# Performance work log

Measured on AMD Instinct MI355X. Metric: run time of the kernel, lower is better.

## Reference

```python
import jax, jax.numpy as jnp
import numpy as np

N, E, IN_DIM, OUT_DIM, NNZ = 4096, 2048, 256, 256, 65536
ALPHA = 0.2          # LeakyReLU negative slope
NEG_GAT = -9e15      # masked_fill value for GAT adjacency mask
NEG_ATT = -1e9       # masked_fill value inside ScaledDotProductAttention_hyper


def setup_inputs() -> dict:
    key = jax.random.key(0)
    ks = jax.random.split(key, 10)
    stdv = 1.0 / np.sqrt(OUT_DIM)
    u = lambda k, shape: jax.random.uniform(k, shape, jnp.float32, -stdv, stdv)
    x = jax.random.normal(ks[0], (N, IN_DIM), jnp.float32)
    node_idx = jax.random.randint(ks[1], (NNZ,), 0, N, jnp.int32)
    edge_idx = jax.random.randint(ks[2], (NNZ,), 0, E, jnp.int32)
    hyperedge_index = jnp.stack([node_idx, edge_idx])  # [2, NNZ]
    return {
        "x": x,
        "weight": u(ks[3], (IN_DIM, OUT_DIM)),
        "weight2": u(ks[4], (IN_DIM, OUT_DIM)),
        "weight3": u(ks[5], (OUT_DIM, OUT_DIM)),
        "weight_g": u(ks[6], (IN_DIM, OUT_DIM)),
        "a_g": u(ks[7], (2 * OUT_DIM, 1)),
        "word_context": u(ks[8], (1, OUT_DIM)),
        "bias": u(ks[9], (OUT_DIM,)),
        "hyperedge_index": hyperedge_index,
        "num_edges": E,
    }


def reference(x, weight, weight2, weight3, weight_g, a_g, word_context, bias,
              hyperedge_index, num_edges):
    n = x.shape[0]
    d = weight_g.shape[1]
    temp = d ** 0.5  # temperature = out_features ** 0.5

    # --- hypergraph preprocessing: dense incidence H [N, E] and node adjacency A [N, N]
    H = jnp.zeros((n, num_edges), x.dtype).at[hyperedge_index[0], hyperedge_index[1]].set(1.0)
    A = (H @ H.T > 0).astype(x.dtype)
    A = A.at[jnp.arange(n), jnp.arange(n)].set(1.0)  # fill_diagonal_(1)

    # --- dense GAT-style attention over the clique-expanded graph
    Wh_g = x @ weight_g                               # [N, D]
    Wh1 = Wh_g @ a_g[:d]                              # [N, 1]
    Wh2 = Wh_g @ a_g[d:]                              # [N, 1]
    e_g = jax.nn.leaky_relu(Wh1 + Wh2.T, ALPHA)       # [N, N]
    attention_g = jax.nn.softmax(jnp.where(A > 0, e_g, NEG_GAT), axis=1)

    # --- project node-node attention onto hyperedges: [N, E]
    graph2hyper = attention_g @ H

    # --- dual hypergraph cross-attention (eval mode: dropout is identity)
    x_4att = x @ weight2                              # [N, D]
    xw = x @ weight + bias                            # [N, D] (transfer=True)

    # attention1: hyperedge queries attend over nodes, mask = H.T [E, N]
    q1 = jnp.broadcast_to(word_context[0], (num_edges, d))
    attn1 = (q1 / temp) @ x_4att.T                    # [E, N]
    attn1 = jnp.where(H.T == 0, NEG_ATT, attn1)
    att1 = jax.nn.softmax(graph2hyper.T, axis=-1) + jax.nn.softmax(attn1, axis=-1)
    edge = att1 @ xw                                  # [E, D]
    att2he = att1.T                                   # [N, E]

    # attention2: node queries attend over hyperedges, mask = H [N, E]
    edge_4att = edge @ weight3                        # [E, D]
    attn2 = (x_4att / temp) @ edge_4att.T             # [N, E]
    attn2 = jnp.where(H == 0, NEG_ATT, attn2)
    att2hn = jax.nn.softmax(graph2hyper, axis=-1) + jax.nn.softmax(attn2, axis=-1)
    node = att2hn @ edge                              # [N, D]

    # --- combine attentions and aggregate
    att2_he_out = att2he @ att2he.T                   # [N, N]
    att2_hn_out = att2hn @ att2hn.T                   # [N, N]
    attention_out = attention_g + att2_he_out + att2_hn_out
    h_prime_g = jax.nn.elu(attention_out @ Wh_g)      # concat=True -> ELU

    node = jax.nn.relu(node)                          # concat=True -> ReLU, then squeeze
    return node, h_prime_g
```

## Files before the change

### kernel.cpp

```cpp
#include <hip/hip_runtime.h>
#include <cstdint>
#include <cstddef>


#define DI __device__ __forceinline__
typedef unsigned short u16;
typedef unsigned char  u8;
typedef unsigned int   u32;
typedef __bf16 bf16x8 __attribute__((ext_vector_type(8)));
typedef float  f32x4  __attribute__((ext_vector_type(4)));
typedef u32    u32x4  __attribute__((ext_vector_type(4)));
typedef int    i32x4  __attribute__((ext_vector_type(4)));
typedef int    i32x8  __attribute__((ext_vector_type(8)));

constexpr int NN  = 4096;
constexpr int EE  = 2048;
constexpr int NNZb = 65536;

constexpr size_t MB = (size_t)1 << 20;
constexpr size_t OFF_HBITS   = 0;
constexpr size_t OFF_HBITST  = 1*MB;
constexpr size_t OFF_ABITS   = 2*MB;
constexpr size_t OFF_EDGE    = 2*MB;
constexpr size_t OFF_WH1     = 4*MB;
constexpr size_t OFF_WH2     = 4*MB + 16384;
constexpr size_t OFF_V       = 4*MB + 32768;
constexpr size_t OFF_RSINV   = 4*MB + 49152;
constexpr size_t OFF_WCAT    = 5*MB;
constexpr size_t OFF_XB      = 6*MB;
constexpr size_t OFF_EDGET   = 6*MB;
constexpr size_t OFF_HN2T    = 7*MB;
constexpr size_t OFF_WHG     = 8*MB;
constexpr size_t OFF_X4ATT   = 10*MB;
constexpr size_t OFF_YB      = 12*MB;
constexpr size_t OFF_XWT     = 14*MB;
constexpr size_t OFF_WHGTA   = 16*MB;
constexpr size_t OFF_HBT     = 18*MB;
constexpr size_t OFF_EDGE2T  = 18*MB;
constexpr size_t OFF_WHGTB   = 26*MB;
constexpr size_t OFF_EXPA    = 36*MB;
constexpr size_t OFF_ATT1    = 36*MB;
constexpr size_t OFF_ATT2HN  = 36*MB;
constexpr size_t OFF_ATT1T   = 52*MB;
constexpr size_t OFF_G2H     = 68*MB;
constexpr size_t OFF_G2HT    = 84*MB;
constexpr size_t OFF_ATT2HNT = 84*MB;
constexpr size_t OFF_ATTN2   = 100*MB;
constexpr size_t OFF_G1      = 116*MB;
constexpr size_t OFF_C2      = 120*MB;
constexpr size_t OFF_HN2ACC  = 124*MB;

DI u16 to_bf(float f) {
  union { float f; u32 u; } x; x.f = f;
  u32 r = x.u + 0x7fffu + ((x.u >> 16) & 1u);
  return (u16)(r >> 16);
}
DI float from_bf(u16 h) { union { u32 u; float f; } x; x.u = (u32)h << 16; return x.f; }
DI void store_bf4(u16* p, float a, float b, float c, float d) {
  u32 lo = (u32)to_bf(a) | ((u32)to_bf(b) << 16);
  u32 hi = (u32)to_bf(c) | ((u32)to_bf(d) << 16);
  *(u32*)p = lo; *((u32*)p + 1) = hi;
}
DI u32 pack_fp8x4(float a, float b, float c, float d) {
  int p = __builtin_amdgcn_cvt_pk_fp8_f32(a, b, 0, false);
  p = __builtin_amdgcn_cvt_pk_fp8_f32(c, d, p, true);
  return (u32)p;
}

DI float wredf(float v) {
  #pragma unroll
  for (int o = 32; o; o >>= 1) v += __shfl_down(v, o);
  return v;
}
DI int wredi(int v) {
  #pragma unroll
  for (int o = 32; o; o >>= 1) v += __shfl_down(v, o);
  return v;
}

typedef __attribute__((address_space(3))) void lds_void;
typedef __attribute__((address_space(1))) void glb_void;
DI void async_load16(const void* g, void* l) {
  __builtin_amdgcn_global_load_lds((glb_void*)(uintptr_t)g,
                                   (lds_void*)(u32)(uintptr_t)l, 16, 0, 0);
}

template <int BM, int BN, class Epi>
DI void gemm_body(const u16* __restrict__ A, const u16* __restrict__ B,
                  int nb, int K, int k0, int kLen, Epi epi, int tile,
                  u16* As, u16* Bs)
{
  constexpr int BK = 64;
  constexpr int WM = BM / 2, WN = BN / 2;
  constexpr int FM = WM / 16, FN = WN / 16;
  constexpr int AI = (BM * 8) / 256, BI = (BN * 8) / 256;

  const int tid = threadIdx.x;
  const int w = tid >> 6, l = tid & 63;
  const int bi = tile / nb, bj = tile - bi * nb;
  const int i0 = bi * BM, j0 = bj * BN;
  const int wm = (w & 1) * WM, wn = (w >> 1) * WN;
  const int quad = l >> 4, m16 = l & 15;

  f32x4 acc[FM][FN] = {};

  for (int kb = k0; kb < k0 + kLen; kb += BK) {
    __syncthreads();
    #pragma unroll
    for (int i = 0; i < AI; ++i) {
      const int ci = (i * 4 + w) * 64 + l;
      const int r = ci >> 3;
      const int lc = (ci & 7) ^ (r & 7);
      async_load16(A + (size_t)(i0 + r) * K + kb + lc * 8, &As[(i * 4 + w) * 512]);
    }
    #pragma unroll
    for (int i = 0; i < BI; ++i) {
      const int ci = (i * 4 + w) * 64 + l;
      const int r = ci >> 3;
      const int lc = (ci & 7) ^ (r & 7);
      async_load16(B + (size_t)(j0 + r) * K + kb + lc * 8, &Bs[(i * 4 + w) * 512]);
    }
    __syncthreads();
    #pragma unroll
    for (int ks = 0; ks < 2; ++ks) {
      bf16x8 af[FM], bfv[FN];
      #pragma unroll
      for (int mi = 0; mi < FM; ++mi) {
        const int row = wm + mi * 16 + m16;
        af[mi] = *(const bf16x8*)&As[row * BK + (((ks * 4 + quad) ^ (row & 7)) * 8)];
      }
      #pragma unroll
      for (int ni = 0; ni < FN; ++ni) {
        const int row = wn + ni * 16 + m16;
        bfv[ni] = *(const bf16x8*)&Bs[row * BK + (((ks * 4 + quad) ^ (row & 7)) * 8)];
      }
      #pragma unroll
      for (int mi = 0; mi < FM; ++mi)
        #pragma unroll
        for (int ni = 0; ni < FN; ++ni)
          acc[mi][ni] = __builtin_amdgcn_mfma_f32_16x16x32_bf16(
              af[mi], bfv[ni], acc[mi][ni], 0, 0, 0);
    }
  }
  #pragma unroll
  for (int mi = 0; mi < FM; ++mi)
    #pragma unroll
    for (int ni = 0; ni < FN; ++ni) {
      const int rb = i0 + wm + mi * 16 + quad * 4;
      const int c  = j0 + wn + ni * 16 + m16;
      epi(rb, c, acc[mi][ni]);
    }
}

DI void t32_tile(const u16* __restrict__ in, u16* __restrict__ out,
                 int R, int C, int bx, int by, u16* t) {
  int tx = threadIdx.x & 31, ty = threadIdx.x >> 5;
  int x0 = bx * 32, y0 = by * 32;
  #pragma unroll
  for (int k = 0; k < 32; k += 8)
    t[(ty + k) * 33 + tx] = in[(size_t)(y0 + ty + k) * C + x0 + tx];
  __syncthreads();
  #pragma unroll
  for (int k = 0; k < 32; k += 8)
    out[(size_t)(x0 + ty + k) * R + y0 + tx] = t[tx * 33 + ty + k];
}

struct EpiG0 {
  u16 *whg, *whgTa, *x4, *xwT; u8* whgTb; const float* bias;
  DI void operator()(int r, int c, f32x4 v) const {
    if (c < 256) {
      #pragma unroll
      for (int i = 0; i < 4; ++i) whg[(r + i) * 256 + c] = to_bf(v[i]);
      store_bf4(&whgTa[(size_t)c * NN + r], v[0], v[1], v[2], v[3]);
      *(u32*)&whgTb[(size_t)c * NN + r] = pack_fp8x4(v[0], v[1], v[2], v[3]);
    } else if (c < 512) {
      #pragma unroll
      for (int i = 0; i < 4; ++i) x4[(r + i) * 256 + (c - 256)] = to_bf(v[i]);
    } else {
      float b = bias[c - 512];
      store_bf4(&xwT[(size_t)(c - 512) * NN + r], v[0]+b, v[1]+b, v[2]+b, v[3]+b);
    }
  }
};
struct EpiBig {
  const float* rsInv; u16* g2h; u16* g2hT; float* g1;
  DI void operator()(int r, int c, f32x4 v) const {
    float w0 = v[0]*rsInv[r], w1 = v[1]*rsInv[r+1], w2 = v[2]*rsInv[r+2], w3 = v[3]*rsInv[r+3];
    if (c < 2048) {
      g2h[(size_t)r * EE + c] = to_bf(w0);
      g2h[(size_t)(r+1) * EE + c] = to_bf(w1);
      g2h[(size_t)(r+2) * EE + c] = to_bf(w2);
      g2h[(size_t)(r+3) * EE + c] = to_bf(w3);
      store_bf4(&g2hT[(size_t)c * NN + r], w0, w1, w2, w3);
    } else {
      g1[(r) * 256 + (c - 2048)] = w0;
      g1[(r+1) * 256 + (c - 2048)] = w1;
      g1[(r+2) * 256 + (c - 2048)] = w2;
      g1[(r+3) * 256 + (c - 2048)] = w3;
    }
  }
};
struct EpiEdgeT {
  u16 *edgeT, *edge2T, *edge;
  DI void operator()(int r, int c, f32x4 v) const {
    if (r < 256) {
      #pragma unroll
      for (int i = 0; i < 4; ++i) edgeT[(size_t)(r + i) * EE + c] = to_bf(v[i]);
      store_bf4(&edge[(size_t)c * 256 + r], v[0], v[1], v[2], v[3]);
    } else {
      #pragma unroll
      for (int i = 0; i < 4; ++i) edge2T[(size_t)(r - 256 + i) * EE + c] = to_bf(v[i]);
    }
  }
};
struct EpiCombine {
  const float* g1; const float* c2; float* out;
  DI void operator()(int r, int c, f32x4 v) const {
    if (c < 256) {
      #pragma unroll
      for (int i = 0; i < 4; ++i) out[(r + i) * 256 + c] = fmaxf(v[i], 0.f);
    } else {
      int d = c - 256;
      #pragma unroll
      for (int i = 0; i < 4; ++i) {
        float s = g1[(r + i) * 256 + d] + c2[(r + i) * 256 + d] + v[i];
        out[1048576 + (r + i) * 256 + d] = s > 0.f ? s : expm1f(s);
      }
    }
  }
};
struct EpiBf16 { u16* out; int ldn;
  DI void operator()(int r, int c, f32x4 v) const {
    #pragma unroll
    for (int i = 0; i < 4; ++i) out[(size_t)(r + i) * ldn + c] = to_bf(v[i]);
  } };
struct EpiBf16Scale { u16* out; int ldn; float s;
  DI void operator()(int r, int c, f32x4 v) const {
    #pragma unroll
    for (int i = 0; i < 4; ++i) out[(size_t)(r + i) * ldn + c] = to_bf(v[i] * s);
  } };
struct EpiF32 { float* out; int ldn;
  DI void operator()(int r, int c, f32x4 v) const {
    #pragma unroll
    for (int i = 0; i < 4; ++i) out[(size_t)(r + i) * ldn + c] = v[i];
  } };
struct EpiAtomF32 { float* out; int ldn;
  DI void operator()(int r, int c, f32x4 v) const {
    #pragma unroll
    for (int i = 0; i < 4; ++i) atomicAdd(&out[(size_t)(r + i) * ldn + c], v[i]);
  } };

template <int BM, int BN, int S, int LB, class Epi>
__global__ __launch_bounds__(256, LB)
void gemm_k(const u16* __restrict__ A, const u16* __restrict__ B,
            int nb, int K, Epi epi) {
  __shared__ __align__(16) u16 smem[(BM + BN) * 64];
  int t = blockIdx.x;
  int k0 = 0, kLen = K;
  if (S > 1) {
    const int tilesPer = gridDim.x / S;
    const int s = t / tilesPer; t -= s * tilesPer;
    kLen = K / S; k0 = s * kLen;
  }
  gemm_body<BM, BN>(A, B, nb, K, k0, kLen, epi, t, smem, smem + BM * 64);
}

template <class Epi>
__global__ __launch_bounds__(256, 3)
void gemm_mx(const u8* __restrict__ A, const u8* __restrict__ B,
             int nb, int K, Epi epi) {
  constexpr int BM = 128, BN = 96, BK = 128;
  constexpr int FM = 4, FN = 3;
  __shared__ __align__(16) u8 As[BM * BK];
  __shared__ __align__(16) u8 Bs[BN * BK];

  const int tid = threadIdx.x;
  const int w = tid >> 6, l = tid & 63;
  const int tile = blockIdx.x;
  const int bi = tile / nb, bj = tile - bi * nb;
  const int i0 = bi * BM, j0 = bj * BN;
  const int wm = (w & 1) * 64, wn = (w >> 1) * 48;
  const int quad = l >> 4, m16 = l & 15;

  f32x4 acc[FM][FN] = {};

  for (int kb = 0; kb < K; kb += BK) {
    __syncthreads();
    #pragma unroll
    for (int i = 0; i < 4; ++i) {
      const int ci = (i * 4 + w) * 64 + l;
      const int r = ci >> 3;
      const int lc = (ci & 7) ^ (r & 7);
      async_load16(A + (size_t)(i0 + r) * K + kb + lc * 16, &As[(i * 4 + w) * 1024]);
    }
    #pragma unroll
    for (int i = 0; i < 3; ++i) {
      const int ci = (i * 4 + w) * 64 + l;
      const int r = ci >> 3;
      const int lc = (ci & 7) ^ (r & 7);
      async_load16(B + (size_t)(j0 + r) * K + kb + lc * 16, &Bs[(i * 4 + w) * 1024]);
    }
    __syncthreads();
    i32x8 af[FM], bf[FN];
    #pragma unroll
    for (int mi = 0; mi < FM; ++mi) {
      const int row = wm + mi * 16 + m16;
      const i32x4 lo = *(const i32x4*)&As[row * BK + ((quad * 2) ^ (row & 7)) * 16];
      const i32x4 hi = *(const i32x4*)&As[row * BK + ((quad * 2 + 1) ^ (row & 7)) * 16];
      af[mi][0] = lo[0]; af[mi][1] = lo[1]; af[mi][2] = lo[2]; af[mi][3] = lo[3];
      af[mi][4] = hi[0]; af[mi][5] = hi[1]; af[mi][6] = hi[2]; af[mi][7] = hi[3];
    }
    #pragma unroll
    for (int ni = 0; ni < FN; ++ni) {
      const int row = wn + ni * 16 + m16;
      const i32x4 lo = *(const i32x4*)&Bs[row * BK + ((quad * 2) ^ (row & 7)) * 16];
      const i32x4 hi = *(const i32x4*)&Bs[row * BK + ((quad * 2 + 1) ^ (row & 7)) * 16];
      bf[ni][0] = lo[0]; bf[ni][1] = lo[1]; bf[ni][2] = lo[2]; bf[ni][3] = lo[3];
      bf[ni][4] = hi[0]; bf[ni][5] = hi[1]; bf[ni][6] = hi[2]; bf[ni][7] = hi[3];
    }
    #pragma unroll
    for (int mi = 0; mi < FM; ++mi)
      #pragma unroll
      for (int ni = 0; ni < FN; ++ni)
        acc[mi][ni] = __builtin_amdgcn_mfma_scale_f32_16x16x128_f8f6f4(
            af[mi], bf[ni], acc[mi][ni], 0, 0,
            0, 0x7F7F7F7F, 0, 0x7F7F7F7F);
  }
  #pragma unroll
  for (int mi = 0; mi < FM; ++mi)
    #pragma unroll
    for (int ni = 0; ni < FN; ++ni) {
      const int rb = i0 + wm + mi * 16 + quad * 4;
      const int c  = j0 + wn + ni * 16 + m16;
      epi(rb, c, acc[mi][ni]);
    }
}

__global__ void k_prep(const float* wg, const float* w2, const float* w1,
                       const float* w3, const float* x, u16* wcat, u16* xb,
                       char* zbits, char* zhbt, char* zhn2) {
  int idx = blockIdx.x * 256 + threadIdx.x;
  if (blockIdx.x < 5120) {
    if (idx < 196608) {
      int blk = idx >> 16, r = idx & 65535;
      int d = r >> 8, kk = r & 255;
      const float* src = blk == 0 ? wg : blk == 1 ? w2 : w1;
      wcat[idx] = to_bf(src[kk * 256 + d]);
    } else if (idx < 262144) {
      int r = idx - 196608;
      wcat[196608 + r] = to_bf(w3[r]);
    } else {
      int r = idx - 262144;
      xb[r] = to_bf(x[r]);
    }
  } else {
    int z = idx - 5120 * 256;
    u32x4 zero = {0, 0, 0, 0};
    if (z < 262144)      ((u32x4*)zbits)[z] = zero;
    else if (z < 786432) ((u32x4*)zhbt)[z - 262144] = zero;
    else                 ((u32x4*)zhn2)[z - 786432] = zero;
  }
}

__global__ void k_scatter_diag(const int* __restrict__ hidx, u32* hbits, u32* hbitsT,
                               u8* hbT, u32* abits) {
  int k = blockIdx.x * 256 + threadIdx.x;
  if (k < NNZb) {
    int n = hidx[k], e = hidx[NNZb + k];
    atomicOr(&hbits[n * 64 + (e >> 5)], 1u << (e & 31));
    atomicOr(&hbitsT[e * 128 + (n >> 5)], 1u << (n & 31));
    hbT[(size_t)e * NN + n] = 0x38;
  } else {
    int i = k - NNZb;
    if (i < NN) atomicOr(&abits[i * 128 + (i >> 5)], 1u << (i & 31));
  }
}

__global__ void k_rowclique(const u16* __restrict__ whg, const u16* __restrict__ x4,
                            const float* __restrict__ ag, const float* __restrict__ wc,
                            float* wh1, float* wh2, float* v,
                            const u32* __restrict__ hbitsT, u32* abits) {
  __shared__ int list[512];
  __shared__ int cnt;
  int tid = threadIdx.x;
  if (blockIdx.x < 1024) {
    int wv = tid >> 6, l = tid & 63;
    int row = blockIdx.x * 4 + wv;
    float s1 = 0, s2 = 0, s3 = 0;
    #pragma unroll
    for (int dd = 0; dd < 4; ++dd) {
      int d = l * 4 + dd;
      float a = from_bf(whg[row * 256 + d]);
      s1 += a * ag[d]; s2 += a * ag[256 + d];
      s3 += from_bf(x4[row * 256 + d]) * wc[d];
    }
    s1 = wredf(s1); s2 = wredf(s2); s3 = wredf(s3);
    if (l == 0) { wh1[row] = s1; wh2[row] = s2; v[row] = s3 * (1.0f / 16.0f); }
  } else {
    int e = blockIdx.x - 1024;
    if (tid == 0) cnt = 0;
    __syncthreads();
    if (tid < 128) {
      u32 w = hbitsT[e * 128 + tid];
      while (w) {
        int b = __ffs(w) - 1;
        int p = atomicAdd(&cnt, 1);
        if (p < 512) list[p] = tid * 32 + b;
        w &= w - 1;
      }
    }
    __syncthreads();
    int c = cnt < 512 ? cnt : 512;
    for (int p = tid; p < c * c; p += 256) {
      int i = list[p / c], j = list[p % c];
      atomicOr(&abits[i * 128 + (j >> 5)], 1u << (j & 31));
    }
  }
}

__global__ void k_exprows(const u32* __restrict__ abits, const float* __restrict__ wh1,
                          const float* __restrict__ wh2, u8* __restrict__ expA,
                          float* rsInv) {
  int i = blockIdx.x, tid = threadIdx.x;
  __shared__ float w2s[NN];
  __shared__ float ssum;
  for (int j = tid; j < NN; j += 256) w2s[j] = wh2[j];
  if (tid == 0) ssum = 0.f;
  __syncthreads();
  float a = wh1[i], lsum = 0.f;
  #pragma unroll
  for (int it = 0; it < 4; ++it) {
    int j = it * 1024 + tid * 4;
    u32 w = abits[i * 128 + (j >> 5)];
    u32 m = (w >> (j & 31)) & 0xFu;
    float x0 = 0.f, x1 = 0.f, x2 = 0.f, x3 = 0.f;
    if (m & 1u) { float z = a + w2s[j];     float eg = z > 0.f ? z : 0.2f * z; x0 = __expf(eg); }
    if (m & 2u) { float z = a + w2s[j + 1]; float eg = z > 0.f ? z : 0.2f * z; x1 = __expf(eg); }
    if (m & 4u) { float z = a + w2s[j + 2]; float eg = z > 0.f ? z : 0.2f * z; x2 = __expf(eg); }
    if (m & 8u) { float z = a + w2s[j + 3]; float eg = z > 0.f ? z : 0.2f * z; x3 = __expf(eg); }
    u32 word = pack_fp8x4(x0, x1, x2, x3);
    *(u32*)&expA[(size_t)i * NN + j] = word;
    lsum += __builtin_amdgcn_cvt_f32_fp8(word, 0) + __builtin_amdgcn_cvt_f32_fp8(word, 1)
          + __builtin_amdgcn_cvt_f32_fp8(word, 2) + __builtin_amdgcn_cvt_f32_fp8(word, 3);
  }
  lsum = wredf(lsum);
  if ((tid & 63) == 0) atomicAdd(&ssum, lsum);
  __syncthreads();
  if (tid == 0) rsInv[i] = 1.0f / ssum;
}

__global__ void k_edge_softmax(const u16* __restrict__ g2hT, const u32* __restrict__ hbitsT,
                               const float* __restrict__ v, u16* __restrict__ att1) {
  int e = blockIdx.x, tid = threadIdx.x;
  __shared__ float evals[NN];
  __shared__ u32 hw[128];
  __shared__ float s1s, s2s; __shared__ int cs;
  if (tid == 0) { s1s = 0.f; s2s = 0.f; cs = 0; }
  if (tid < 128) hw[tid] = hbitsT[e * 128 + tid];
  __syncthreads();
  float sum1 = 0.f;
  for (int j = tid; j < NN; j += 256) {
    float ev = __expf(from_bf(g2hT[(size_t)e * NN + j]));
    evals[j] = ev; sum1 += ev;
  }
  float sum2 = 0.f; int cnt = 0;
  if (tid < 128) {
    u32 w = hw[tid]; cnt = __popc(w);
    while (w) { int b = __ffs(w) - 1; sum2 += __expf(v[tid * 32 + b]); w &= w - 1; }
  }
  sum1 = wredf(sum1); sum2 = wredf(sum2); cnt = wredi(cnt);
  if ((tid & 63) == 0) { atomicAdd(&s1s, sum1); atomicAdd(&s2s, sum2); atomicAdd(&cs, cnt); }
  __syncthreads();
  float inv1 = 1.0f / s1s;
  int c = cs;
  float inv2 = c > 0 ? 1.0f / s2s : 0.0f;
  float unif = c > 0 ? 0.0f : (1.0f / (float)NN);
  for (int j = tid; j < NN; j += 256) {
    float t = evals[j] * inv1 + unif;
    if ((hw[j >> 5] >> (j & 31)) & 1) t += __expf(v[j]) * inv2;
    att1[(size_t)e * NN + j] = to_bf(t);
  }
}

__global__ __launch_bounds__(256, 2)
void k_tri_edge(const u16* __restrict__ Fcat, const u16* __restrict__ Att1,
                EpiEdgeT e0,
                const u16* __restrict__ X4att, const u16* __restrict__ W3b,
                EpiBf16 e1,
                const u16* __restrict__ tin, u16* __restrict__ tout) {
  __shared__ __align__(16) u16 smem[192 * 64];
  int b = blockIdx.x;
  if (b < 256) {
    const int xcd = b & 7, idx = b >> 3;
    const int t = (idx / 4) * 32 + xcd * 4 + (idx & 3);
    gemm_body<64, 64>(Fcat, Att1, 32, NN, 0, NN, e0, t, smem, smem + 64 * 64);
  }
  else if (b < 384) gemm_body<128, 64>(X4att, W3b, 4, 256, 0, 256, e1, b - 256, smem, smem + 128 * 64);
  else { int t = b - 384; t32_tile(tin, tout, EE, NN, t & 127, t >> 7, smem); }
}

__global__ __launch_bounds__(256, 2)
void k_dual_attn2(const u16* __restrict__ Att1T, const u16* __restrict__ Edge2T,
                  EpiF32 e0,
                  const u16* __restrict__ Yb, const u16* __restrict__ Edge,
                  EpiBf16Scale e1) {
  __shared__ __align__(16) u16 smem[256 * 64];
  int b = blockIdx.x;
  if (b < 128) gemm_body<128, 64>(Att1T, Edge2T, 4, EE, 0, EE, e0, b, smem, smem + 128 * 64);
  else         gemm_body<128, 128>(Yb, Edge, 16, 256, 0, 256, e1, b - 128, smem, smem + 128 * 64);
}

__global__ void k_node_softmax(const u16* __restrict__ g2h, const u16* __restrict__ attn2,
                               const u32* __restrict__ hbits, u16* __restrict__ att2hn) {
  int n = blockIdx.x, tid = threadIdx.x;
  __shared__ float ev3[EE], ev4[EE];
  __shared__ u32 hw[64];
  __shared__ float s3s, s4s; __shared__ int cs;
  if (tid == 0) { s3s = 0.f; s4s = 0.f; cs = 0; }
  if (tid < 64) hw[tid] = hbits[n * 64 + tid];
  __syncthreads();
  float s3 = 0.f, s4 = 0.f; int cl = 0;
  for (int e = tid; e < EE; e += 256) {
    float x3 = __expf(from_bf(g2h[(size_t)n * EE + e]));
    ev3[e] = x3; s3 += x3;
    bool m = (hw[e >> 5] >> (e & 31)) & 1;
    float x4 = m ? __expf(from_bf(attn2[(size_t)n * EE + e])) : 0.f;
    ev4[e] = x4; s4 += x4; cl += m;
  }
  s3 = wredf(s3); s4 = wredf(s4); cl = wredi(cl);
  if ((tid & 63) == 0) { atomicAdd(&s3s, s3); atomicAdd(&s4s, s4); atomicAdd(&cs, cl); }
  __syncthreads();
  float inv3 = 1.0f / s3s;
  int c = cs;
  float inv4 = c > 0 ? 1.0f / s4s : 0.0f;
  float unif = c > 0 ? 0.0f : (1.0f / (float)EE);
  for (int e = tid; e < EE; e += 256)
    att2hn[(size_t)n * EE + e] = to_bf(ev3[e] * inv3 + ev4[e] * inv4 + unif);
}

__global__ void k_transpose(const u16* __restrict__ in, u16* __restrict__ out,
                            int R, int C) {
  __shared__ u16 t[32 * 33];
  t32_tile(in, out, R, C, blockIdx.x, blockIdx.y, t);
}

__global__ void k_cast_hn2(const float* __restrict__ acc, u16* __restrict__ hn2T) {
  int idx = blockIdx.x * 256 + threadIdx.x;
  hn2T[idx] = to_bf(acc[idx]);
}

extern "C" void kernel_launch(void* const* d_in, const int* in_sizes, int n_in,
                              void* d_out, int out_size, void* d_ws, size_t ws_size,
                              hipStream_t stream) {
  (void)in_sizes; (void)n_in; (void)out_size; (void)ws_size;
  const float* x    = (const float*)d_in[0];
  const float* w1   = (const float*)d_in[1];
  const float* w2   = (const float*)d_in[2];
  const float* w3   = (const float*)d_in[3];
  const float* wg   = (const float*)d_in[4];
  const float* ag   = (const float*)d_in[5];
  const float* wc   = (const float*)d_in[6];
  const float* bias = (const float*)d_in[7];
  const int*   hidx = (const int*)d_in[8];
  float* out = (float*)d_out;
  char* ws = (char*)d_ws;

  u32* Hbits   = (u32*)(ws + OFF_HBITS);
  u32* HbitsT  = (u32*)(ws + OFF_HBITST);
  u32* Abits   = (u32*)(ws + OFF_ABITS);
  float* Wh1   = (float*)(ws + OFF_WH1);
  float* Wh2   = (float*)(ws + OFF_WH2);
  float* V     = (float*)(ws + OFF_V);
  float* RsInv = (float*)(ws + OFF_RSINV);
  u16* Wcat    = (u16*)(ws + OFF_WCAT);
  u16* W3b     = Wcat + 196608;
  u16* Xb      = (u16*)(ws + OFF_XB);
  u16* Whg     = (u16*)(ws + OFF_WHG);
  u16* X4att   = (u16*)(ws + OFF_X4ATT);
  u16* Yb      = (u16*)(ws + OFF_YB);
  u16* XwT     = (u16*)(ws + OFF_XWT);
  u16* WhgTa   = (u16*)(ws + OFF_WHGTA);
  u8*  HbT8    = (u8*)(ws + OFF_HBT);
  u8*  WhgTb8  = (u8*)(ws + OFF_WHGTB);
  u8*  ExpA8   = (u8*)(ws + OFF_EXPA);
  u16* Att1    = (u16*)(ws + OFF_ATT1);
  u16* Att1T   = (u16*)(ws + OFF_ATT1T);
  u16* Att2hn  = (u16*)(ws + OFF_ATT2HN);
  u16* G2h     = (u16*)(ws + OFF_G2H);
  u16* G2hT    = (u16*)(ws + OFF_G2HT);
  u16* Att2hnT = (u16*)(ws + OFF_ATT2HNT);
  u16* Attn2   = (u16*)(ws + OFF_ATTN2);
  float* G1    = (float*)(ws + OFF_G1);
  float* C2    = (float*)(ws + OFF_C2);
  float* Hn2Acc = (float*)(ws + OFF_HN2ACC);
  u16* Edge    = (u16*)(ws + OFF_EDGE);
  u16* EdgeT   = (u16*)(ws + OFF_EDGET);
  u16* Hn2T    = (u16*)(ws + OFF_HN2T);
  u16* Edge2T  = (u16*)(ws + OFF_EDGE2T);

  k_prep<<<8704, 256, 0, stream>>>(wg, w2, w1, w3, x, Wcat, Xb,
                                   ws + OFF_HBITS, ws + OFF_HBT, ws + OFF_HN2ACC);
  k_scatter_diag<<<272, 256, 0, stream>>>(hidx, Hbits, HbitsT, HbT8, Abits);
  gemm_k<128, 64, 1, 3><<<384, 256, 0, stream>>>(
      Xb, Wcat, 12, 256, EpiG0{Whg, WhgTa, X4att, XwT, WhgTb8, bias});
  k_rowclique<<<3072, 256, 0, stream>>>(Whg, X4att, ag, wc, Wh1, Wh2, V,
                                        HbitsT, Abits);
  k_exprows<<<NN, 256, 0, stream>>>(Abits, Wh1, Wh2, ExpA8, RsInv);
  gemm_mx<<<768, 256, 0, stream>>>(
      ExpA8, HbT8, 24, NN, EpiBig{RsInv, G2h, G2hT, G1});
  k_edge_softmax<<<EE, 256, 0, stream>>>(G2hT, HbitsT, V, Att1);
  k_tri_edge<<<8576, 256, 0, stream>>>(
      XwT, Att1, EpiEdgeT{EdgeT, Edge2T, Edge},
      X4att, W3b, EpiBf16{Yb, 256},
      Att1, Att1T);
  k_dual_attn2<<<640, 256, 0, stream>>>(
      Att1T, Edge2T, EpiF32{C2, 256},
      Yb, Edge, EpiBf16Scale{Attn2, EE, 1.0f / 16.0f});
  k_node_softmax<<<NN, 256, 0, stream>>>(G2h, Attn2, Hbits, Att2hn);
  k_transpose<<<dim3(64, 128), 256, 0, stream>>>(Att2hn, Att2hnT, NN, EE);
  gemm_k<64, 64, 4, 3><<<512, 256, 0, stream>>>(
      WhgTa, Att2hnT, 32, NN, EpiAtomF32{Hn2Acc, EE});
  k_cast_hn2<<<2048, 256, 0, stream>>>(Hn2Acc, Hn2T);
  gemm_k<64, 64, 1, 2><<<512, 256, 0, stream>>>(
      Att2hn, EdgeT, 8, EE, EpiCombine{G1, C2, out});
}
```

Measured before the change: 345.3 us.

## Compute attn2 only at incidence nonzeros and read wh2 directly in exprows

The dense NxE GEMM that produced attn2 is replaced by a sparse path. Each wavefront owns one hyperedge, walks its transposed incidence bits and computes a dot product only for member nodes, writing the scaled scores just at those positions. Masked entries of attn2 are left unwritten, which is safe only if k_node_softmax never reads them. Separately, k_exprows drops its shared-memory staging of wh2 and does vectorized global loads instead. The sparse loop trades MFMA throughput for far fewer FLOPs, but with irregular serial per-bit iterations and scattered 2-byte stores.

Result: slower. 362.7 us (+5.0%).

```diff
diff --git a/kernel.cpp b/kernel.cpp
--- a/kernel.cpp
+++ b/kernel.cpp
@@ -234,11 +234,6 @@
     #pragma unroll
     for (int i = 0; i < 4; ++i) out[(size_t)(r + i) * ldn + c] = to_bf(v[i]);
   } };
-struct EpiBf16Scale { u16* out; int ldn; float s;
-  DI void operator()(int r, int c, f32x4 v) const {
-    #pragma unroll
-    for (int i = 0; i < 4; ++i) out[(size_t)(r + i) * ldn + c] = to_bf(v[i] * s);
-  } };
 struct EpiF32 { float* out; int ldn;
   DI void operator()(int r, int c, f32x4 v) const {
     #pragma unroll
@@ -422,9 +417,7 @@
                           const float* __restrict__ wh2, u8* __restrict__ expA,
                           float* rsInv) {
   int i = blockIdx.x, tid = threadIdx.x;
-  __shared__ float w2s[NN];
   __shared__ float ssum;
-  for (int j = tid; j < NN; j += 256) w2s[j] = wh2[j];
   if (tid == 0) ssum = 0.f;
   __syncthreads();
   float a = wh1[i], lsum = 0.f;
@@ -433,11 +426,12 @@
     int j = it * 1024 + tid * 4;
     u32 w = abits[i * 128 + (j >> 5)];
     u32 m = (w >> (j & 31)) & 0xFu;
+    const f32x4 wv = *(const f32x4*)&wh2[j];
     float x0 = 0.f, x1 = 0.f, x2 = 0.f, x3 = 0.f;
-    if (m & 1u) { float z = a + w2s[j];     float eg = z > 0.f ? z : 0.2f * z; x0 = __expf(eg); }
-    if (m & 2u) { float z = a + w2s[j + 1]; float eg = z > 0.f ? z : 0.2f * z; x1 = __expf(eg); }
-    if (m & 4u) { float z = a + w2s[j + 2]; float eg = z > 0.f ? z : 0.2f * z; x2 = __expf(eg); }
-    if (m & 8u) { float z = a + w2s[j + 3]; float eg = z > 0.f ? z : 0.2f * z; x3 = __expf(eg); }
+    if (m & 1u) { float z = a + wv[0]; float eg = z > 0.f ? z : 0.2f * z; x0 = __expf(eg); }
+    if (m & 2u) { float z = a + wv[1]; float eg = z > 0.f ? z : 0.2f * z; x1 = __expf(eg); }
+    if (m & 4u) { float z = a + wv[2]; float eg = z > 0.f ? z : 0.2f * z; x2 = __expf(eg); }
+    if (m & 8u) { float z = a + wv[3]; float eg = z > 0.f ? z : 0.2f * z; x3 = __expf(eg); }
     u32 word = pack_fp8x4(x0, x1, x2, x3);
     *(u32*)&expA[(size_t)i * NN + j] = word;
     lsum += __builtin_amdgcn_cvt_f32_fp8(word, 0) + __builtin_amdgcn_cvt_f32_fp8(word, 1)
@@ -500,14 +494,38 @@
 }
 
 __global__ __launch_bounds__(256, 2)
-void k_dual_attn2(const u16* __restrict__ Att1T, const u16* __restrict__ Edge2T,
-                  EpiF32 e0,
-                  const u16* __restrict__ Yb, const u16* __restrict__ Edge,
-                  EpiBf16Scale e1) {
-  __shared__ __align__(16) u16 smem[256 * 64];
+void k_dual_c2sp(const u16* __restrict__ Att1T, const u16* __restrict__ Edge2T,
+                 EpiF32 e0,
+                 const u16* __restrict__ Yb, const u16* __restrict__ Edge,
+                 const u32* __restrict__ hbitsT, u16* __restrict__ attn2) {
+  __shared__ __align__(16) u16 smem[192 * 64];
   int b = blockIdx.x;
-  if (b < 128) gemm_body<128, 64>(Att1T, Edge2T, 4, EE, 0, EE, e0, b, smem, smem + 128 * 64);
-  else         gemm_body<128, 128>(Yb, Edge, 16, 256, 0, 256, e1, b - 128, smem, smem + 128 * 64);
+  if (b < 128) {
+    gemm_body<128, 64>(Att1T, Edge2T, 4, EE, 0, EE, e0, b, smem, smem + 128 * 64);
+    return;
+  }
+  const int w = threadIdx.x >> 6, l = threadIdx.x & 63;
+  const int e = (b - 128) * 4 + w;
+  f32x4 er;
+  {
+    const u32* ep = (const u32*)&Edge[(size_t)e * 256 + l * 4];
+    u32 p0 = ep[0], p1 = ep[1];
+    er[0] = from_bf((u16)p0); er[1] = from_bf((u16)(p0 >> 16));
+    er[2] = from_bf((u16)p1); er[3] = from_bf((u16)(p1 >> 16));
+  }
+  for (int wd = 0; wd < 128; ++wd) {
+    u32 bits = hbitsT[e * 128 + wd];
+    while (bits) {
+      const int bit = __ffs(bits) - 1; bits &= bits - 1;
+      const int n = wd * 32 + bit;
+      const u32* yp = (const u32*)&Yb[(size_t)n * 256 + l * 4];
+      u32 q0 = yp[0], q1 = yp[1];
+      float s = from_bf((u16)q0) * er[0] + from_bf((u16)(q0 >> 16)) * er[1]
+              + from_bf((u16)q1) * er[2] + from_bf((u16)(q1 >> 16)) * er[3];
+      s = wredf(s);
+      if (l == 0) attn2[(size_t)n * EE + e] = to_bf(s * (1.0f / 16.0f));
+    }
+  }
 }
 
 __global__ void k_node_softmax(const u16* __restrict__ g2h, const u16* __restrict__ attn2,
@@ -613,9 +631,9 @@
       XwT, Att1, EpiEdgeT{EdgeT, Edge2T, Edge},
       X4att, W3b, EpiBf16{Yb, 256},
       Att1, Att1T);
-  k_dual_attn2<<<640, 256, 0, stream>>>(
+  k_dual_c2sp<<<640, 256, 0, stream>>>(
       Att1T, Edge2T, EpiF32{C2, 256},
-      Yb, Edge, EpiBf16Scale{Attn2, EE, 1.0f / 16.0f});
+      Yb, Edge, HbitsT, Attn2);
   k_node_softmax<<<NN, 256, 0, stream>>>(G2h, Attn2, Hbits, Att2hn);
   k_transpose<<<dim3(64, 128), 256, 0, stream>>>(Att2hn, Att2hnT, NN, EE);
   gemm_k<64, 64, 4, 3><<<512, 256, 0, stream>>>(
```
